# Optimization experiments

Hardware: AMD Instinct MI355X
Metric: run time of the kernel (lower is better)

The kernel has to match this reference:

```python
import jax, jax.numpy as jnp
import numpy as np
from jax import lax

T_SIZE = 8        # frames
S_SIZE = 14       # spatial grid side
N_HEAD = 16
D_MODEL = 1024
L = S_SIZE * S_SIZE          # 196 patch tokens per frame
N_BATCH = 8


def _layernorm(x, g, b):
    # torch LayerNorm subclass computes in fp32 then casts back
    x32 = x.astype(jnp.float32)
    m = x32.mean(-1, keepdims=True)
    v = x32.var(-1, keepdims=True)
    return ((x32 - m) * lax.rsqrt(v + 1e-5) * g + b).astype(x.dtype)


def _mha(x, wqkv, bqkv, wo, bo, bias):
    # x: [S, B, C] seq-first like torch MHA; bias: [n_head, S, S] or None
    S, B, C = x.shape
    hd = C // N_HEAD
    qkv = x @ wqkv.T + bqkv
    q, k, v = jnp.split(qkv, 3, axis=-1)
    def h(t):
        return t.reshape(S, B, N_HEAD, hd).transpose(1, 2, 0, 3)  # [B,H,S,hd]
    q = h(q) * (1.0 / np.sqrt(hd))
    k, v = h(k), h(v)
    scores = jnp.einsum('bhqd,bhkd->bhqk', q, k)
    if bias is not None:
        scores = scores + bias[None]  # broadcast over batch (torch repeats; same math)
    a = jax.nn.softmax(scores, axis=-1)
    o = jnp.einsum('bhqk,bhkd->bhqd', a, v).transpose(2, 0, 1, 3).reshape(S, B, C)
    return o @ wo.T + bo


def _rel_idx():
    t = jnp.arange(T_SIZE)
    idx_t = t[:, None] - t[None, :] + T_SIZE - 1          # [T,T]
    c = jnp.arange(L)
    qi, qj = c // S_SIZE, c % S_SIZE
    i_off = qi[:, None] - qi[None, :] + S_SIZE - 1
    j_off = qj[:, None] - qj[None, :] + S_SIZE - 1
    idx_s = i_off * (2 * S_SIZE - 1) + j_off              # [L,L]
    return idx_t, idx_s


def reference(x, pos_w, pos_b, ln_t_g, ln_t_b, rpb_t, wqkv_t, bqkv_t, wo_t, bo_t,
              ln1_g, ln1_b, rpb_s, wqkv_s, bqkv_s, wo_s, bo_s,
              ln2_g, ln2_b, fc_w, fc_b, proj_w, proj_b):
    T, S, H, C = T_SIZE, S_SIZE, N_HEAD, D_MODEL
    LT = L * T
    N = x.shape[1]
    idx_t, idx_s = _rel_idx()

    # depthwise 3D conv positional embedding on patch tokens (token order is (h w t))
    v = x[1:].reshape(S, S, T, N, C).transpose(3, 4, 2, 0, 1)  # [N,C,T,H,W]
    conv = lax.conv_general_dilated(
        v, pos_w, (1, 1, 1), [(1, 1), (1, 1), (1, 1)],
        dimension_numbers=('NCDHW', 'OIDHW', 'NCDHW'),
        feature_group_count=C) + pos_b[None, :, None, None, None]
    tmp = (v + conv).reshape(N, C, T, L).transpose(3, 2, 0, 1).reshape(LT, N, C)
    x = jnp.concatenate([x[:1], tmp], 0)

    # temporal attention: '(l t) n c -> t (n l) c'
    xt = x[1:].reshape(L, T, N, C).transpose(1, 2, 0, 3).reshape(T, N * L, C)
    bias_t = rpb_t[idx_t].transpose(2, 0, 1)  # [H,T,T]
    rt = _mha(_layernorm(xt, ln_t_g, ln_t_b), wqkv_t, bqkv_t, wo_t, bo_t, bias_t)
    rt = rt.reshape(T, N, L, C).transpose(2, 0, 1, 3).reshape(LT, N, C)
    xt_full = x[1:] + rt

    # spatial attention with replicated cls token: 'l (t n) c' batching
    cls = jnp.tile(x[:1], (1, T, 1))                      # [1, T*N, C], t-major
    xs = jnp.concatenate([cls, xt_full.reshape(L, T * N, C)], 0)  # [L+1, T*N, C]
    bias_s = jnp.zeros((H, L + 1, L + 1), x.dtype).at[:, 1:, 1:].set(
        rpb_s[idx_s].transpose(2, 0, 1))
    rs = _mha(_layernorm(xs, ln1_g, ln1_b), wqkv_s, bqkv_s, wo_s, bo_s, bias_s)
    cls_out = rs[0].reshape(T, N, C).mean(0, keepdims=True)       # mean over frames
    spa = rs[1:].reshape(LT, N, C)                                # 'l (t n) -> (l t) n'
    x = x + jnp.concatenate([cls_out, spa], 0)

    # MLP with QuickGELU
    h = _layernorm(x, ln2_g, ln2_b) @ fc_w.T + fc_b
    h = h * jax.nn.sigmoid(1.702 * h)
    return x + (h @ proj_w.T + proj_b)


def setup_inputs() -> dict:
    key = jax.random.key(0)
    ks = jax.random.split(key, 12)
    C = D_MODEL
    f32 = jnp.float32
    def w(k, shape, s=0.02):
        return jax.random.normal(k, shape, f32) * s
    return {
        'x': jax.random.normal(ks[0], (1 + L * T_SIZE, N_BATCH, C), f32),
        'pos_w': w(ks[1], (C, 1, 3, 3, 3)),
        'pos_b': jnp.zeros((C,), f32),
        'ln_t_g': jnp.ones((C,), f32), 'ln_t_b': jnp.zeros((C,), f32),
        'rpb_t': w(ks[2], (2 * T_SIZE - 1, N_HEAD)),
        'wqkv_t': w(ks[3], (3 * C, C)), 'bqkv_t': jnp.zeros((3 * C,), f32),
        'wo_t': w(ks[4], (C, C)), 'bo_t': jnp.zeros((C,), f32),
        'ln1_g': jnp.ones((C,), f32), 'ln1_b': jnp.zeros((C,), f32),
        'rpb_s': w(ks[5], ((2 * S_SIZE - 1) ** 2, N_HEAD)),
        'wqkv_s': w(ks[6], (3 * C, C)), 'bqkv_s': jnp.zeros((3 * C,), f32),
        'wo_s': w(ks[7], (C, C)), 'bo_s': jnp.zeros((C,), f32),
        'ln2_g': jnp.ones((C,), f32), 'ln2_b': jnp.zeros((C,), f32),
        'fc_w': w(ks[8], (4 * C, C)), 'fc_b': jnp.zeros((4 * C,), f32),
        'proj_w': w(ks[9], (C, 4 * C)), 'proj_b': jnp.zeros((C,), f32),
    }
```

## Files before the change

### kernel.cpp

```cpp
#include <hip/hip_runtime.h>
#include <stdint.h>

typedef unsigned short u16;
typedef __attribute__((ext_vector_type(8))) __bf16 bf16x8;
typedef __attribute__((ext_vector_type(4))) float f32x4;

__device__ __forceinline__ float bf2f(u16 u) {
    return __uint_as_float(((unsigned int)u) << 16);
}
__device__ __forceinline__ u16 f2bf(float f) {
    unsigned int u = __float_as_uint(f);
    u += 0x7fffu + ((u >> 16) & 1u);
    return (u16)(u >> 16);
}

__device__ __forceinline__ void gl16(const u16* g, u16* l) {
    __builtin_amdgcn_global_load_lds(
        (const __attribute__((address_space(1))) unsigned int*)(uintptr_t)g,
        (__attribute__((address_space(3))) unsigned int*)(uintptr_t)l,
        16, 0, 0);
}

__global__ __launch_bounds__(256) void cvt_bf16(const float4* __restrict__ in,
                                                ushort4* __restrict__ out, int n4) {
    int tid = blockIdx.x * 256 + threadIdx.x;
    if (tid < n4) {
        float4 v = in[tid];
        ushort4 o;
        o.x = f2bf(v.x); o.y = f2bf(v.y); o.z = f2bf(v.z); o.w = f2bf(v.w);
        out[tid] = o;
    }
}

__global__ __launch_bounds__(256) void cvt_wt(const float* __restrict__ pw,
                                              float* __restrict__ wt) {
    int tid = blockIdx.x * 256 + threadIdx.x;
    if (tid < 27648) {
        int tap = tid >> 10, c = tid & 1023;
        wt[tid] = pw[c * 27 + tap];
    }
}

__global__ __launch_bounds__(256) void posembed(const float4* __restrict__ x4,
                                                const float4* __restrict__ wt4,
                                                const float4* __restrict__ pb4,
                                                float4* __restrict__ out4) {
    int tid = blockIdx.x * 256 + threadIdx.x;
    float4 xv = x4[tid];
    int rf = tid >> 11;
    if (rf == 0) { out4[tid] = xv; return; }
    int c4 = tid & 255;
    int n = (tid >> 8) & 7;
    int r = rf - 1;
    int t = r & 7, l = r >> 3;
    int i = l / 14, j = l - i * 14;
    float4 pbv = pb4[c4];
    float a0 = xv.x + pbv.x, a1 = xv.y + pbv.y, a2 = xv.z + pbv.z, a3 = xv.w + pbv.w;
#pragma unroll
    for (int dt = 0; dt < 3; dt++) {
        int tt = t + dt - 1;
        if (tt < 0 || tt > 7) continue;
#pragma unroll
        for (int di = 0; di < 3; di++) {
            int ii = i + di - 1;
            if (ii < 0 || ii > 13) continue;
#pragma unroll
            for (int dj = 0; dj < 3; dj++) {
                int jj = j + dj - 1;
                if (jj < 0 || jj > 13) continue;
                float4 w4 = wt4[(dt * 9 + di * 3 + dj) * 256 + c4];
                float4 v = x4[(size_t)(1 + ((ii * 14 + jj) << 3) + tt) * 2048 + (n << 8) + c4];
                a0 += w4.x * v.x; a1 += w4.y * v.y; a2 += w4.z * v.z; a3 += w4.w * v.w;
            }
        }
    }
    out4[tid] = (float4){a0, a1, a2, a3};
}

__global__ __launch_bounds__(256) void ln_kernel(const float* __restrict__ resid,
                                                 const u16* __restrict__ Radd,
                                                 const float* __restrict__ g,
                                                 const float* __restrict__ bb,
                                                 u16* __restrict__ out, int mode) {
    int ro = blockIdx.x;
    int tid = threadIdx.x;
    int src, n;
    long long rarow = -1;
    if (mode == 0) {
        int t = ro / 1568, b2 = ro - t * 1568;
        n = b2 / 196;
        int l = b2 - n * 196;
        src = 1 + l * 8 + t;
    } else if (mode == 1) {
        int s = ro >> 6, u = ro & 63;
        int t = u >> 3;
        n = u & 7;
        if (s == 0) src = 0;
        else { src = 1 + (s - 1) * 8 + t; rarow = (long long)(t * 1568 + n * 196 + (s - 1)); }
    } else {
        src = ro >> 3;
        n = ro & 7;
    }
    const float* xp = resid + ((size_t)src * 8 + n) * 1024 + tid * 4;
    float4 xv = *(const float4*)xp;
    float x0 = xv.x, x1 = xv.y, x2 = xv.z, x3 = xv.w;
    if (rarow >= 0) {
        const u16* rp = Radd + rarow * 1024 + tid * 4;
        x0 += bf2f(rp[0]); x1 += bf2f(rp[1]); x2 += bf2f(rp[2]); x3 += bf2f(rp[3]);
    }
    float s1 = x0 + x1 + x2 + x3;
    float s2 = x0 * x0 + x1 * x1 + x2 * x2 + x3 * x3;
#pragma unroll
    for (int off = 32; off > 0; off >>= 1) {
        s1 += __shfl_down(s1, off);
        s2 += __shfl_down(s2, off);
    }
    __shared__ float red[8];
    int lane = tid & 63, w = tid >> 6;
    if (lane == 0) { red[w] = s1; red[4 + w] = s2; }
    __syncthreads();
    float S1 = red[0] + red[1] + red[2] + red[3];
    float S2 = red[4] + red[5] + red[6] + red[7];
    float mean = S1 * (1.f / 1024.f);
    float var = S2 * (1.f / 1024.f) - mean * mean;
    float rstd = rsqrtf(var + 1e-5f);
    int c = tid * 4;
    u16* op = out + (size_t)ro * 1024 + c;
    op[0] = f2bf((x0 - mean) * rstd * g[c + 0] + bb[c + 0]);
    op[1] = f2bf((x1 - mean) * rstd * g[c + 1] + bb[c + 1]);
    op[2] = f2bf((x2 - mean) * rstd * g[c + 2] + bb[c + 2]);
    op[3] = f2bf((x3 - mean) * rstd * g[c + 3] + bb[c + 3]);
}

__global__ __launch_bounds__(512) void gemm256(const u16* __restrict__ A,
                                               const u16* __restrict__ W,
                                               const float* __restrict__ bias,
                                               u16* __restrict__ Co,
                                               int M, int N, int K, int gelu,
                                               int nnt) {
    __shared__ __align__(16) u16 sA[2][16384];
    __shared__ __align__(16) u16 sB[2][16384];
    int tid = threadIdx.x;
    int wid = tid >> 6, lane = tid & 63;
    int wr = wid >> 2, wc = wid & 3;
    int lm = lane & 15, q = lane >> 4;

    int nwg = gridDim.x, orig = blockIdx.x;
    int qq = nwg >> 3, rr = nwg & 7, xcd = orig & 7, blk = orig >> 3;
    int wg = (xcd < rr ? xcd * (qq + 1) : rr * (qq + 1) + (xcd - rr) * qq) + blk;
    int n0 = (wg % nnt) * 256, m0 = (wg / nnt) * 256;

    int NT = K >> 6, NTm1 = NT - 1;

    int rl = wid * 8 + (lane >> 3);
    int cl = ((lane & 7) ^ (rl & 7)) * 8;
    const u16* pA[4];
    const u16* pB[4];
#pragma unroll
    for (int h2 = 0; h2 < 4; h2++) {
        int ra = m0 + h2 * 64 + rl; if (ra > M - 1) ra = M - 1;
        int rb = n0 + h2 * 64 + rl; if (rb > N - 1) rb = N - 1;
        pA[h2] = A + (size_t)ra * K + cl;
        pB[h2] = W + (size_t)rb * K + cl;
    }
    int ldst = wid * 512;

    f32x4 acc[8][4];
#pragma unroll
    for (int i = 0; i < 8; i++)
#pragma unroll
        for (int j = 0; j < 4; j++) acc[i][j] = (f32x4){0.f, 0.f, 0.f, 0.f};

    bf16x8 af[4][2];
    bf16x8 bfv[4][2];

#define STG(P, D, b, h, kt) do { \
        int _k = (kt); if (_k > NTm1) _k = NTm1; \
        gl16(P[(h) * 2] + (size_t)_k * 64, &D[b][(h) * 8192 + ldst]); \
        gl16(P[(h) * 2 + 1] + (size_t)_k * 64, &D[b][(h) * 8192 + 4096 + ldst]); \
    } while (0)
#define LDA_(b, ih) do { \
        _Pragma("unroll") for (int iq = 0; iq < 4; iq++) \
        _Pragma("unroll") for (int kk = 0; kk < 2; kk++) \
            af[iq][kk] = *(const bf16x8*)&sA[b][((ih) * 128 + wr * 64 + iq * 16 + lm) * 64 + \
                                                (((q + kk * 4) ^ (lm & 7)) * 8)]; \
    } while (0)
#define LDB_(b, jh) do { \
        _Pragma("unroll") for (int jq = 0; jq < 2; jq++) \
        _Pragma("unroll") for (int kk = 0; kk < 2; kk++) \
            bfv[(jh) * 2 + jq][kk] = *(const bf16x8*)&sB[b][((jh) * 128 + wc * 32 + jq * 16 + lm) * 64 + \
                                                            (((q + kk * 4) ^ (lm & 7)) * 8)]; \
    } while (0)
#define MMA_(ih, jh) do { \
        __builtin_amdgcn_s_setprio(1); \
        _Pragma("unroll") for (int iq = 0; iq < 4; iq++) \
        _Pragma("unroll") for (int jq = 0; jq < 2; jq++) \
        _Pragma("unroll") for (int kk = 0; kk < 2; kk++) \
            acc[(ih) * 4 + iq][(jh) * 2 + jq] = __builtin_amdgcn_mfma_f32_16x16x32_bf16( \
                af[iq][kk], bfv[(jh) * 2 + jq][kk], acc[(ih) * 4 + iq][(jh) * 2 + jq], 0, 0, 0); \
        __builtin_amdgcn_s_setprio(0); \
    } while (0)
#define BAR __builtin_amdgcn_s_barrier()
#define LGKM0 asm volatile("s_waitcnt lgkmcnt(0)" ::: "memory")
#define VM6 asm volatile("s_waitcnt vmcnt(6)" ::: "memory")

    STG(pA, sA, 0, 0, 0);
    STG(pA, sA, 0, 1, 0);
    STG(pB, sB, 0, 0, 0);
    STG(pB, sB, 0, 1, 0);
    STG(pA, sA, 1, 0, 1);
    STG(pB, sB, 1, 1, 1);
    STG(pA, sA, 1, 1, 1);
    VM6;
    BAR;

    int S = NT >> 1;
    for (int s = 0; s < S; s++) {
        int t = s * 2;
        LDA_(0, 0); LDB_(0, 0);
        STG(pB, sB, 1, 0, t + 1);
        BAR; LGKM0; MMA_(0, 0); BAR;
        LDB_(0, 1);
        STG(pA, sA, 0, 0, t + 2);
        BAR; LGKM0; MMA_(0, 1); BAR;
        LDA_(0, 1);
        STG(pB, sB, 0, 1, t + 2);
        BAR; LGKM0; MMA_(1, 1); BAR;
        STG(pA, sA, 0, 1, t + 2);
        VM6;
        BAR; MMA_(1, 0); BAR;
        LDA_(1, 0); LDB_(1, 0);
        STG(pB, sB, 0, 0, t + 2);
        BAR; LGKM0; MMA_(0, 0); BAR;
        LDB_(1, 1);
        STG(pA, sA, 1, 0, t + 3);
        BAR; LGKM0; MMA_(0, 1); BAR;
        LDA_(1, 1);
        STG(pB, sB, 1, 1, t + 3);
        BAR; LGKM0; MMA_(1, 1); BAR;
        STG(pA, sA, 1, 1, t + 3);
        VM6;
        BAR; MMA_(1, 0); BAR;
    }
    asm volatile("s_waitcnt vmcnt(0)" ::: "memory");

#pragma unroll
    for (int ih = 0; ih < 2; ih++)
#pragma unroll
        for (int iq = 0; iq < 4; iq++) {
            int row_b = m0 + ih * 128 + wr * 64 + iq * 16 + q * 4;
#pragma unroll
            for (int jh = 0; jh < 2; jh++)
#pragma unroll
                for (int jq = 0; jq < 2; jq++) {
                    int col = n0 + jh * 128 + wc * 32 + jq * 16 + lm;
                    float bv = bias[col];
#pragma unroll
                    for (int r = 0; r < 4; r++) {
                        int row = row_b + r;
                        if (row < M) {
                            float v = acc[ih * 4 + iq][jh * 2 + jq][r] + bv;
                            if (gelu) v = v / (1.f + __expf(-1.702f * v));
                            Co[(size_t)row * N + col] = f2bf(v);
                        }
                    }
                }
        }
#undef STG
#undef LDA_
#undef LDB_
#undef MMA_
#undef BAR
#undef LGKM0
#undef VM6
}

__global__ __launch_bounds__(64) void attn_t(const u16* __restrict__ qkv,
                                             const float* __restrict__ rpb,
                                             u16* __restrict__ out) {
    int blk = blockIdx.x;
    int b = blk % 1568, h = blk / 1568;
    int d = threadIdx.x;
    __shared__ float qs[8][65], ks[8][65], vs[8][65];
    __shared__ float ps[8][9];
#pragma unroll
    for (int t = 0; t < 8; t++) {
        size_t row = (size_t)(t * 1568 + b) * 3072 + h * 64 + d;
        qs[t][d] = bf2f(qkv[row]) * 0.125f;
        ks[t][d] = bf2f(qkv[row + 1024]);
        vs[t][d] = bf2f(qkv[row + 2048]);
    }
    __syncthreads();
    int tq = d >> 3, tk = d & 7;
    float s = rpb[(tq - tk + 7) * 16 + h];
#pragma unroll
    for (int dd = 0; dd < 64; dd++) s += qs[tq][dd] * ks[tk][dd];
    float mx = s;
    mx = fmaxf(mx, __shfl_xor(mx, 1));
    mx = fmaxf(mx, __shfl_xor(mx, 2));
    mx = fmaxf(mx, __shfl_xor(mx, 4));
    float p = __expf(s - mx);
    float su = p;
    su += __shfl_xor(su, 1);
    su += __shfl_xor(su, 2);
    su += __shfl_xor(su, 4);
    ps[tq][tk] = p / su;
    __syncthreads();
#pragma unroll
    for (int t2 = 0; t2 < 8; t2++) {
        float o = 0.f;
#pragma unroll
        for (int k2 = 0; k2 < 8; k2++) o += ps[t2][k2] * vs[k2][d];
        out[(size_t)(t2 * 1568 + b) * 1024 + h * 64 + d] = f2bf(o);
    }
}

#define KLS 72
#define PVS 232
__global__ __launch_bounds__(256) void attn_s(const u16* __restrict__ qkv,
                                              const float* __restrict__ rpb,
                                              u16* __restrict__ out) {
    __shared__ u16 Kl[208 * KLS];
    __shared__ u16 Vt[64 * PVS];
    __shared__ u16 Pl[4][16 * PVS];
    __shared__ float rpb_l[736];
    int blk = blockIdx.x;
    int u = blk & 63, h = blk >> 6;
    int tid = threadIdx.x;
    int w = tid >> 6, lane = tid & 63;
    int lm = lane & 15, quad = lane >> 4;

    for (int idx = tid; idx < 197 * 8; idx += 256) {
        int s = idx >> 3, c8 = idx & 7;
        const u16* gp = qkv + (size_t)(s * 64 + u) * 3072 + h * 64 + c8 * 8;
        uint4 kv = *(const uint4*)(gp + 1024);
        uint4 vv = *(const uint4*)(gp + 2048);
        *(uint4*)&Kl[s * KLS + c8 * 8] = kv;
        const u16* vp = (const u16*)&vv;
#pragma unroll
        for (int j = 0; j < 8; j++) Vt[(c8 * 8 + j) * PVS + s] = vp[j];
    }
    for (int i = tid; i < 11 * KLS; i += 256) Kl[197 * KLS + i] = 0;
    for (int i = tid; i < 64 * 35; i += 256) {
        int dd = i / 35, c = 197 + (i - dd * 35);
        Vt[dd * PVS + c] = 0;
    }
    {
        for (int i = lane; i < 256; i += 64) {
            int r = i >> 4, c = 208 + (i & 15);
            Pl[w][r * PVS + c] = 0;
        }
    }
    for (int i = tid; i < 729; i += 256) rpb_l[i] = rpb[i * 16 + h];
    __syncthreads();

    for (int it = 0; it < 4; it++) {
        int qt = it * 4 + w;
        bool act = qt < 13;
        f32x4 sc[13];
        float rs[4];
        if (act) {
            int qrow = qt * 16 + lm;
            int srq = qrow > 196 ? 196 : qrow;
            const u16* qp = qkv + (size_t)(srq * 64 + u) * 3072 + h * 64 + quad * 8;
            bf16x8 aq0 = *(const bf16x8*)qp;
            bf16x8 aq1 = *(const bf16x8*)(qp + 32);
            for (int kt = 0; kt < 13; kt++) {
                bf16x8 bk0 = *(const bf16x8*)&Kl[(kt * 16 + lm) * KLS + quad * 8];
                bf16x8 bk1 = *(const bf16x8*)&Kl[(kt * 16 + lm) * KLS + 32 + quad * 8];
                f32x4 s = __builtin_amdgcn_mfma_f32_16x16x32_bf16(aq0, bk0, (f32x4){0.f, 0.f, 0.f, 0.f}, 0, 0, 0);
                sc[kt] = __builtin_amdgcn_mfma_f32_16x16x32_bf16(aq1, bk1, s, 0, 0, 0);
            }
            int tk = lm;
#pragma unroll
            for (int r = 0; r < 4; r++) {
                int qr = qt * 16 + quad * 4 + r;
                int qcl = qr > 196 ? 196 : qr;
                int lq = qcl - 1;
                int qi = lq / 14, qj = lq - qi * 14;
                for (int kt = 0; kt < 13; kt++) {
                    int tkk = kt * 16 + tk;
                    float v;
                    if (tkk >= 197) v = -1e30f;
                    else {
                        v = sc[kt][r] * 0.125f;
                        if (qr >= 1 && tkk >= 1) {
                            int lk = tkk - 1;
                            int ki = lk / 14, kj = lk - ki * 14;
                            v += rpb_l[(qi - ki + 13) * 27 + (qj - kj + 13)];
                        }
                    }
                    sc[kt][r] = v;
                }
                float mx = -3e38f;
                for (int kt = 0; kt < 13; kt++) mx = fmaxf(mx, sc[kt][r]);
                mx = fmaxf(mx, __shfl_xor(mx, 1));
                mx = fmaxf(mx, __shfl_xor(mx, 2));
                mx = fmaxf(mx, __shfl_xor(mx, 4));
                mx = fmaxf(mx, __shfl_xor(mx, 8));
                float sm = 0.f;
                for (int kt = 0; kt < 13; kt++) {
                    float p = __expf(sc[kt][r] - mx);
                    sc[kt][r] = p;
                    sm += p;
                }
                sm += __shfl_xor(sm, 1);
                sm += __shfl_xor(sm, 2);
                sm += __shfl_xor(sm, 4);
                sm += __shfl_xor(sm, 8);
                rs[r] = sm;
                for (int kt = 0; kt < 13; kt++)
                    Pl[w][(quad * 4 + r) * PVS + kt * 16 + tk] = f2bf(sc[kt][r]);
            }
        }
        __syncthreads();
        if (act) {
            bf16x8 pa[7];
#pragma unroll
            for (int kc = 0; kc < 7; kc++)
                pa[kc] = *(const bf16x8*)&Pl[w][lm * PVS + kc * 32 + quad * 8];
#pragma unroll
            for (int ct = 0; ct < 4; ct++) {
                f32x4 o = (f32x4){0.f, 0.f, 0.f, 0.f};
#pragma unroll
                for (int kc = 0; kc < 7; kc++) {
                    bf16x8 vb = *(const bf16x8*)&Vt[(ct * 16 + lm) * PVS + kc * 32 + quad * 8];
                    o = __builtin_amdgcn_mfma_f32_16x16x32_bf16(pa[kc], vb, o, 0, 0, 0);
                }
#pragma unroll
                for (int r = 0; r < 4; r++) {
                    int qr = qt * 16 + quad * 4 + r;
                    if (qr < 197)
                        out[(size_t)(qr * 64 + u) * 1024 + h * 64 + ct * 16 + lm] =
                            f2bf(o[r] / rs[r]);
                }
            }
        }
        __syncthreads();
    }
}

__global__ __launch_bounds__(256) void add_cls(const u16* __restrict__ R, float4* __restrict__ resid4) {
    int tid = blockIdx.x * 256 + threadIdx.x;
    int c4 = tid & 255, n = tid >> 8;
    float s0 = 0.f, s1 = 0.f, s2 = 0.f, s3 = 0.f;
#pragma unroll
    for (int t = 0; t < 8; t++) {
        ushort4 rv = *(const ushort4*)&R[(size_t)(t * 8 + n) * 1024 + c4 * 4];
        s0 += bf2f(rv.x); s1 += bf2f(rv.y); s2 += bf2f(rv.z); s3 += bf2f(rv.w);
    }
    float4 v = resid4[tid];
    v.x += s0 * 0.125f; v.y += s1 * 0.125f; v.z += s2 * 0.125f; v.w += s3 * 0.125f;
    resid4[tid] = v;
}

__global__ __launch_bounds__(256) void add_spa(const u16* __restrict__ R, float4* __restrict__ resid4) {
    int tid = blockIdx.x * 256 + threadIdx.x;
    int c4 = tid & 255;
    int n = (tid >> 8) & 7;
    int r = tid >> 11;
    int t = r & 7, l = r >> 3;
    int srow = (l + 1) * 64 + t * 8 + n;
    ushort4 rv = *(const ushort4*)&R[(size_t)srow * 1024 + c4 * 4];
    float4 v = resid4[tid + 2048];
    v.x += bf2f(rv.x); v.y += bf2f(rv.y); v.z += bf2f(rv.z); v.w += bf2f(rv.w);
    resid4[tid + 2048] = v;
}

__global__ __launch_bounds__(256) void add_flat(const ushort4* __restrict__ R4, float4* __restrict__ resid4) {
    int tid = blockIdx.x * 256 + threadIdx.x;
    ushort4 rv = R4[tid];
    float4 v = resid4[tid];
    v.x += bf2f(rv.x); v.y += bf2f(rv.y); v.z += bf2f(rv.z); v.w += bf2f(rv.w);
    resid4[tid] = v;
}

extern "C" void kernel_launch(void* const* d_in, const int* in_sizes, int n_in,
                              void* d_out, int out_size, void* d_ws, size_t ws_size,
                              hipStream_t stream) {
    const float* x      = (const float*)d_in[0];
    const float* pos_w  = (const float*)d_in[1];
    const float* pos_b  = (const float*)d_in[2];
    const float* ln_t_g = (const float*)d_in[3];
    const float* ln_t_b = (const float*)d_in[4];
    const float* rpb_t  = (const float*)d_in[5];
    const float* wqkv_t = (const float*)d_in[6];
    const float* bqkv_t = (const float*)d_in[7];
    const float* wo_t   = (const float*)d_in[8];
    const float* bo_t   = (const float*)d_in[9];
    const float* ln1_g  = (const float*)d_in[10];
    const float* ln1_b  = (const float*)d_in[11];
    const float* rpb_s  = (const float*)d_in[12];
    const float* wqkv_s = (const float*)d_in[13];
    const float* bqkv_s = (const float*)d_in[14];
    const float* wo_s   = (const float*)d_in[15];
    const float* bo_s   = (const float*)d_in[16];
    const float* ln2_g  = (const float*)d_in[17];
    const float* ln2_b  = (const float*)d_in[18];
    const float* fc_w   = (const float*)d_in[19];
    const float* fc_b   = (const float*)d_in[20];
    const float* proj_w = (const float*)d_in[21];
    const float* proj_b = (const float*)d_in[22];
    float* resid = (float*)d_out;

    u16* Wq_t  = (u16*)d_ws;
    u16* Wo_t  = Wq_t + 3145728;
    u16* Wq_s  = Wo_t + 1048576;
    u16* Wo_s  = Wq_s + 3145728;
    u16* Wfc   = Wo_s + 1048576;
    u16* Wpj   = Wfc  + 4194304;
    u16* Albuf = Wpj  + 4194304;
    u16* QKV   = Albuf + 12910592;
    u16* Obuf  = QKV   + 38731776;
    u16* Rbuf  = Obuf  + 12910592;
    u16* Hbuf  = QKV;
    float* wt  = (float*)QKV;

    cvt_bf16<<<3072, 256, 0, stream>>>((const float4*)wqkv_t, (ushort4*)Wq_t, 786432);
    cvt_bf16<<<1024, 256, 0, stream>>>((const float4*)wo_t,   (ushort4*)Wo_t, 262144);
    cvt_bf16<<<3072, 256, 0, stream>>>((const float4*)wqkv_s, (ushort4*)Wq_s, 786432);
    cvt_bf16<<<1024, 256, 0, stream>>>((const float4*)wo_s,   (ushort4*)Wo_s, 262144);
    cvt_bf16<<<4096, 256, 0, stream>>>((const float4*)fc_w,   (ushort4*)Wfc,  1048576);
    cvt_bf16<<<4096, 256, 0, stream>>>((const float4*)proj_w, (ushort4*)Wpj,  1048576);
    cvt_wt<<<108, 256, 0, stream>>>(pos_w, wt);

    posembed<<<12552, 256, 0, stream>>>((const float4*)x, (const float4*)wt,
                                        (const float4*)pos_b, (float4*)resid);

    ln_kernel<<<12544, 256, 0, stream>>>(resid, nullptr, ln_t_g, ln_t_b, Albuf, 0);
    gemm256<<<588, 512, 0, stream>>>(Albuf, Wq_t, bqkv_t, QKV, 12544, 3072, 1024, 0, 12);
    attn_t<<<25088, 64, 0, stream>>>(QKV, rpb_t, Obuf);
    gemm256<<<196, 512, 0, stream>>>(Obuf, Wo_t, bo_t, Rbuf, 12544, 1024, 1024, 0, 4);

    ln_kernel<<<12608, 256, 0, stream>>>(resid, Rbuf, ln1_g, ln1_b, Albuf, 1);
    gemm256<<<600, 512, 0, stream>>>(Albuf, Wq_s, bqkv_s, QKV, 12608, 3072, 1024, 0, 12);
    attn_s<<<1024, 256, 0, stream>>>(QKV, rpb_s, Obuf);
    gemm256<<<200, 512, 0, stream>>>(Obuf, Wo_s, bo_s, Rbuf, 12608, 1024, 1024, 0, 4);
    add_cls<<<8, 256, 0, stream>>>(Rbuf, (float4*)resid);
    add_spa<<<12544, 256, 0, stream>>>(Rbuf, (float4*)resid);

    ln_kernel<<<12552, 256, 0, stream>>>(resid, nullptr, ln2_g, ln2_b, Albuf, 2);
    gemm256<<<800, 512, 0, stream>>>(Albuf, Wfc, fc_b, Hbuf, 12552, 4096, 1024, 1, 16);
    gemm256<<<200, 512, 0, stream>>>(Hbuf, Wpj, proj_b, Rbuf, 12552, 1024, 4096, 0, 4);
    add_flat<<<12552, 256, 0, stream>>>((const ushort4*)Rbuf, (float4*)resid);
}
```

Measured before the change: 1.174 ms.

## Use 128x128 GEMM kernel for N=1024 projections and drop explicit lgkm waits

Adds a simpler 128x128-tile, 256-thread bf16 MFMA GEMM with double-buffered direct-to-LDS loads. It is used for the three N=1024 output projections, which launch about 784-792 blocks instead of 196-200 and so fill the 256 CUs better. The 256x256 kernel also drops its explicit lgkmcnt(0) waits in favour of compiler-inserted waits, plus sched_barrier fences. The smaller tiles give less data reuse per block and have no LDS swizzle, so bank conflicts are possible.

```diff
diff --git a/kernel.cpp b/kernel.cpp
--- a/kernel.cpp
+++ b/kernel.cpp
@@ -130,6 +130,88 @@
     op[1] = f2bf((x1 - mean) * rstd * g[c + 1] + bb[c + 1]);
     op[2] = f2bf((x2 - mean) * rstd * g[c + 2] + bb[c + 2]);
     op[3] = f2bf((x3 - mean) * rstd * g[c + 3] + bb[c + 3]);
+}
+
+__global__ __launch_bounds__(256) void gemm_bf16(const u16* __restrict__ A,
+                                                 const u16* __restrict__ W,
+                                                 const float* __restrict__ bias,
+                                                 u16* __restrict__ Co,
+                                                 int M, int N, int K, int gelu,
+                                                 int nx) {
+    __shared__ u16 As[2][128 * 32];
+    __shared__ u16 Bs[2][128 * 32];
+    int tid = threadIdx.x;
+    int T = gridDim.x;
+    int bid = blockIdx.x;
+    int w_ = (bid & 7) * (T >> 3) + (bid >> 3);
+    int n0 = (w_ % nx) * 128;
+    int m0 = (w_ / nx) * 128;
+    int lane = tid & 63, wid = tid >> 6;
+    int wm = (wid >> 1) * 64, wn = (wid & 1) * 64;
+    int lm = lane & 15, q = lane >> 4;
+
+    f32x4 acc[4][4];
+#pragma unroll
+    for (int i = 0; i < 4; i++)
+#pragma unroll
+        for (int j = 0; j < 4; j++) acc[i][j] = (f32x4){0.f, 0.f, 0.f, 0.f};
+
+    int r0 = wid * 32 + (lane >> 2);
+    int colb = (lane & 3) * 8;
+    int mA0 = m0 + r0;          if (mA0 > M - 1) mA0 = M - 1;
+    int mA1 = m0 + r0 + 16;     if (mA1 > M - 1) mA1 = M - 1;
+    const u16* gA0 = A + (size_t)mA0 * K + colb;
+    const u16* gA1 = A + (size_t)mA1 * K + colb;
+    const u16* gB0 = W + (size_t)(n0 + r0) * K + colb;
+    const u16* gB1 = W + (size_t)(n0 + r0 + 16) * K + colb;
+    int wo = wid * 1024;
+
+    auto loadt = [&](int b) {
+        gl16(gA0, &As[b][wo]); gl16(gA1, &As[b][wo + 512]);
+        gl16(gB0, &Bs[b][wo]); gl16(gB1, &Bs[b][wo + 512]);
+        gA0 += 32; gA1 += 32; gB0 += 32; gB1 += 32;
+    };
+    auto comput = [&](int b) {
+        bf16x8 af[4], bfr[4];
+#pragma unroll
+        for (int i = 0; i < 4; i++) af[i] = *(const bf16x8*)&As[b][(wm + i * 16 + lm) * 32 + q * 8];
+#pragma unroll
+        for (int j = 0; j < 4; j++) bfr[j] = *(const bf16x8*)&Bs[b][(wn + j * 16 + lm) * 32 + q * 8];
+#pragma unroll
+        for (int i = 0; i < 4; i++)
+#pragma unroll
+            for (int j = 0; j < 4; j++)
+                acc[i][j] = __builtin_amdgcn_mfma_f32_16x16x32_bf16(af[i], bfr[j], acc[i][j], 0, 0, 0);
+    };
+
+    int Tt = K >> 5;
+    loadt(0);
+    __syncthreads();
+    loadt(1); comput(0); __syncthreads();
+    for (int t = 2; t + 1 < Tt; t += 2) {
+        loadt(0); comput(1); __syncthreads();
+        loadt(1); comput(0); __syncthreads();
+    }
+    comput(1);
+
+#pragma unroll
+    for (int i = 0; i < 4; i++) {
+        int row_b = m0 + wm + i * 16 + q * 4;
+#pragma unroll
+        for (int j = 0; j < 4; j++) {
+            int col = n0 + wn + j * 16 + lm;
+            float bv = bias[col];
+#pragma unroll
+            for (int r = 0; r < 4; r++) {
+                int row = row_b + r;
+                if (row < M) {
+                    float v = acc[i][j][r] + bv;
+                    if (gelu) v = v / (1.f + __expf(-1.702f * v));
+                    Co[(size_t)row * N + col] = f2bf(v);
+                }
+            }
+        }
+    }
 }
 
 __global__ __launch_bounds__(512) void gemm256(const u16* __restrict__ A,
@@ -201,7 +283,7 @@
         __builtin_amdgcn_s_setprio(0); \
     } while (0)
 #define BAR __builtin_amdgcn_s_barrier()
-#define LGKM0 asm volatile("s_waitcnt lgkmcnt(0)" ::: "memory")
+#define SBAR0 __builtin_amdgcn_sched_barrier(0)
 #define VM6 asm volatile("s_waitcnt vmcnt(6)" ::: "memory")
 
     STG(pA, sA, 0, 0, 0);
@@ -212,35 +294,35 @@
     STG(pB, sB, 1, 1, 1);
     STG(pA, sA, 1, 1, 1);
     VM6;
-    BAR;
+    BAR; SBAR0;
 
     int S = NT >> 1;
     for (int s = 0; s < S; s++) {
         int t = s * 2;
         LDA_(0, 0); LDB_(0, 0);
         STG(pB, sB, 1, 0, t + 1);
-        BAR; LGKM0; MMA_(0, 0); BAR;
+        BAR; MMA_(0, 0); BAR;
         LDB_(0, 1);
         STG(pA, sA, 0, 0, t + 2);
-        BAR; LGKM0; MMA_(0, 1); BAR;
+        BAR; MMA_(0, 1); BAR;
         LDA_(0, 1);
         STG(pB, sB, 0, 1, t + 2);
-        BAR; LGKM0; MMA_(1, 1); BAR;
+        BAR; MMA_(1, 1); BAR;
         STG(pA, sA, 0, 1, t + 2);
         VM6;
-        BAR; MMA_(1, 0); BAR;
+        BAR; SBAR0; MMA_(1, 0); BAR;
         LDA_(1, 0); LDB_(1, 0);
         STG(pB, sB, 0, 0, t + 2);
-        BAR; LGKM0; MMA_(0, 0); BAR;
+        BAR; MMA_(0, 0); BAR;
         LDB_(1, 1);
         STG(pA, sA, 1, 0, t + 3);
-        BAR; LGKM0; MMA_(0, 1); BAR;
+        BAR; MMA_(0, 1); BAR;
         LDA_(1, 1);
         STG(pB, sB, 1, 1, t + 3);
-        BAR; LGKM0; MMA_(1, 1); BAR;
+        BAR; MMA_(1, 1); BAR;
         STG(pA, sA, 1, 1, t + 3);
         VM6;
-        BAR; MMA_(1, 0); BAR;
+        BAR; SBAR0; MMA_(1, 0); BAR;
     }
     asm volatile("s_waitcnt vmcnt(0)" ::: "memory");
 
@@ -271,7 +353,7 @@
 #undef LDB_
 #undef MMA_
 #undef BAR
-#undef LGKM0
+#undef SBAR0
 #undef VM6
 }
 
@@ -530,17 +612,17 @@
     ln_kernel<<<12544, 256, 0, stream>>>(resid, nullptr, ln_t_g, ln_t_b, Albuf, 0);
     gemm256<<<588, 512, 0, stream>>>(Albuf, Wq_t, bqkv_t, QKV, 12544, 3072, 1024, 0, 12);
     attn_t<<<25088, 64, 0, stream>>>(QKV, rpb_t, Obuf);
-    gemm256<<<196, 512, 0, stream>>>(Obuf, Wo_t, bo_t, Rbuf, 12544, 1024, 1024, 0, 4);
+    gemm_bf16<<<784, 256, 0, stream>>>(Obuf, Wo_t, bo_t, Rbuf, 12544, 1024, 1024, 0, 8);
 
     ln_kernel<<<12608, 256, 0, stream>>>(resid, Rbuf, ln1_g, ln1_b, Albuf, 1);
     gemm256<<<600, 512, 0, stream>>>(Albuf, Wq_s, bqkv_s, QKV, 12608, 3072, 1024, 0, 12);
     attn_s<<<1024, 256, 0, stream>>>(QKV, rpb_s, Obuf);
-    gemm256<<<200, 512, 0, stream>>>(Obuf, Wo_s, bo_s, Rbuf, 12608, 1024, 1024, 0, 4);
+    gemm_bf16<<<792, 256, 0, stream>>>(Obuf, Wo_s, bo_s, Rbuf, 12608, 1024, 1024, 0, 8);
     add_cls<<<8, 256, 0, stream>>>(Rbuf, (float4*)resid);
     add_spa<<<12544, 256, 0, stream>>>(Rbuf, (float4*)resid);
 
     ln_kernel<<<12552, 256, 0, stream>>>(resid, nullptr, ln2_g, ln2_b, Albuf, 2);
     gemm256<<<800, 512, 0, stream>>>(Albuf, Wfc, fc_b, Hbuf, 12552, 4096, 1024, 1, 16);
-    gemm256<<<200, 512, 0, stream>>>(Hbuf, Wpj, proj_b, Rbuf, 12552, 1024, 4096, 0, 4);
+    gemm_bf16<<<792, 256, 0, stream>>>(Hbuf, Wpj, proj_b, Rbuf, 12552, 1024, 4096, 0, 8);
     add_flat<<<12552, 256, 0, stream>>>((const ushort4*)Rbuf, (float4*)resid);
 }
```

Measured after the change: 1.241 ms. 5.7% more time.
